# Optimization experiments

Measured on AMD Instinct MI355X. Metric: run time of the kernel, lower is better.

## Reference

```python
import jax, jax.numpy as jnp
import numpy as np

HIDDEN = 2048
NUM_HEADS = 16
NUM_KV_HEADS = 16
QK_NOPE = 128
QK_ROPE = 64
HEAD_DIM = QK_NOPE + QK_ROPE  # 192
V_HEAD = 128
KV_LORA = 512
Q_LORA = 1536
EPS = 1e-6


def rmsnorm(x, w):
    var = jnp.mean(x * x, axis=-1, keepdims=True)
    return x * jax.lax.rsqrt(var + EPS) * w


def setup_inputs() -> dict:
    key = jax.random.key(0)
    ks = jax.random.split(key, 8)
    s = lambda fan_in: 1.0 / np.sqrt(fan_in)
    return {
        "hidden_states": jax.random.normal(ks[0], (2, 2048, HIDDEN), jnp.float32),
        # weights stored as [in, out] so forward is x @ W
        "q_a_w": jax.random.normal(ks[1], (HIDDEN, Q_LORA), jnp.float32) * s(HIDDEN),
        "q_a_ln_w": jnp.ones((Q_LORA,), jnp.float32),
        "q_b_w": jax.random.normal(ks[2], (Q_LORA, NUM_HEADS * HEAD_DIM), jnp.float32) * s(Q_LORA),
        "kv_a_w": jax.random.normal(ks[3], (HIDDEN, KV_LORA + NUM_KV_HEADS * QK_ROPE), jnp.float32) * s(HIDDEN),
        "kv_a_ln_w": jnp.ones((KV_LORA,), jnp.float32),
        "kv_b_w": jax.random.normal(ks[4], (KV_LORA, NUM_KV_HEADS * (QK_NOPE + V_HEAD)), jnp.float32) * s(KV_LORA),
        "o_w": jax.random.normal(ks[5], (NUM_HEADS * V_HEAD, HIDDEN), jnp.float32) * s(NUM_HEADS * V_HEAD),
    }


def reference(hidden_states, q_a_w, q_a_ln_w, q_b_w, kv_a_w, kv_a_ln_w, kv_b_w, o_w):
    B, T, _ = hidden_states.shape
    # Q path: low-rank down-proj -> RMSNorm -> up-proj
    q = rmsnorm(hidden_states @ q_a_w, q_a_ln_w) @ q_b_w
    q = q.reshape(B, T, NUM_HEADS, HEAD_DIM)  # [B,T,H,192]

    # KV path: joint down-proj producing latent + rope slice
    kv_raw = hidden_states @ kv_a_w
    kv_latent = rmsnorm(kv_raw[..., :KV_LORA], kv_a_ln_w)
    k_rope = kv_raw[..., KV_LORA:].reshape(B, T, NUM_KV_HEADS, QK_ROPE)
    kv = (kv_latent @ kv_b_w).reshape(B, T, NUM_KV_HEADS, QK_NOPE + V_HEAD)
    k_nope = kv[..., :QK_NOPE]
    v = kv[..., QK_NOPE:]  # [B,T,Hkv,128]

    # NOTE: the original forward computes RoPE cos/sin but never applies the
    # rotation; q_rope/k_rope are used as-is (faithfully reproduced here).
    k = jnp.concatenate([k_nope, k_rope], axis=-1)  # [B,T,Hkv,192]
    # num_kv_groups == 1, so no repeat_interleave needed

    scale = 1.0 / jnp.sqrt(jnp.float32(HEAD_DIM))
    scores = jnp.einsum("bqhd,bkhd->bhqk", q, k) * scale  # [B,H,T,T]
    causal = jnp.tril(jnp.ones((T, T), bool))
    scores = jnp.where(causal, scores, jnp.finfo(scores.dtype).min)
    probs = jax.nn.softmax(scores, axis=-1)
    attn = jnp.einsum("bhqk,bkhd->bqhd", probs, v)  # [B,T,H,128]
    attn = attn.reshape(B, T, NUM_HEADS * V_HEAD)
    return attn @ o_w
```

## Files before the change

kernel.cpp:

```cpp
#include <hip/hip_runtime.h>
#include <cstdint>
#include <cstddef>

typedef unsigned short u16;
typedef short short8 __attribute__((ext_vector_type(8)));
typedef float f32x4 __attribute__((ext_vector_type(4)));

#define B_   2
#define T_   2048
#define H_   16
#define HID_ 2048
#define DQK_ 192
#define DV_  128
#define AW_  3072

__device__ __forceinline__ float bf2f(u16 u) {
  unsigned int v = ((unsigned int)u) << 16;
  return __builtin_bit_cast(float, v);
}
__device__ __forceinline__ u16 f2bf(float f) {
  unsigned int u = __builtin_bit_cast(unsigned int, f);
  u += 0x7fff + ((u >> 16) & 1);
  return (u16)(u >> 16);
}
__device__ __forceinline__ void load_lds16(const void* g, void* l) {
  __builtin_amdgcn_global_load_lds((const __attribute__((address_space(1))) void*)g,
                                   (__attribute__((address_space(3))) void*)l, 16, 0, 0);
}

__global__ __launch_bounds__(256) void cast_f32_bf16(const float* __restrict__ x,
                                                     u16* __restrict__ y) {
  size_t i = ((size_t)blockIdx.x * 256 + threadIdx.x) * 8;
  float4 a = *(const float4*)&x[i];
  float4 b = *(const float4*)&x[i + 4];
  u16 r[8];
  r[0] = f2bf(a.x); r[1] = f2bf(a.y); r[2] = f2bf(a.z); r[3] = f2bf(a.w);
  r[4] = f2bf(b.x); r[5] = f2bf(b.y); r[6] = f2bf(b.z); r[7] = f2bf(b.w);
  *(uint4*)&y[i] = *(const uint4*)&r[0];
}

__global__ __launch_bounds__(256) void transpose_cast_k(const float* __restrict__ W,
                                                        u16* __restrict__ Wt,
                                                        int K, int N) {
  __shared__ u16 tile[32][33];
  int n0 = blockIdx.x * 32, k0 = blockIdx.y * 32;
  int tx = threadIdx.x & 31, ty = threadIdx.x >> 5;
#pragma unroll
  for (int i = 0; i < 32; i += 8)
    tile[ty + i][tx] = f2bf(W[(size_t)(k0 + ty + i) * N + n0 + tx]);
  __syncthreads();
#pragma unroll
  for (int i = 0; i < 32; i += 8)
    Wt[(size_t)(n0 + ty + i) * K + k0 + tx] = tile[tx][ty + i];
}

__global__ __launch_bounds__(256) void rmsnorm_k(const u16* __restrict__ in, int in_stride,
                                                 int L, const float* __restrict__ w,
                                                 u16* __restrict__ out, int out_stride) {
  int row = blockIdx.x;
  const u16* x = in + (size_t)row * in_stride;
  float ss = 0.f;
  for (int i = threadIdx.x * 8; i < L; i += 2048) {
    uint4 v = *(const uint4*)&x[i];
    const u16* p = (const u16*)&v;
#pragma unroll
    for (int e = 0; e < 8; ++e) { float f = bf2f(p[e]); ss += f * f; }
  }
#pragma unroll
  for (int m = 32; m >= 1; m >>= 1) ss += __shfl_xor(ss, m);
  __shared__ float red[4];
  if ((threadIdx.x & 63) == 0) red[threadIdx.x >> 6] = ss;
  __syncthreads();
  ss = red[0] + red[1] + red[2] + red[3];
  float inv = rsqrtf(ss / (float)L + 1e-6f);
  u16* o = out + (size_t)row * out_stride;
  for (int i = threadIdx.x * 8; i < L; i += 2048) {
    uint4 v = *(const uint4*)&x[i];
    const u16* p = (const u16*)&v;
    u16 r8[8];
#pragma unroll
    for (int e = 0; e < 8; ++e) r8[e] = f2bf(bf2f(p[e]) * inv * w[i + e]);
    *(uint4*)&o[i] = *(const uint4*)&r8[0];
  }
}

template <int EPI>
__global__ __launch_bounds__(256) void gemm_bt(const u16* __restrict__ A,
                                               const u16* __restrict__ Bt,
                                               void* __restrict__ Cout,
                                               int M, int N, int K) {
  __shared__ u16 As[128 * 32];
  __shared__ u16 Bs[128 * 32];
  const int nbx = N >> 7;
  const int bx = blockIdx.x % nbx, by = blockIdx.x / nbx;
  const int m0 = by << 7, n0 = bx << 7;
  const int tid = threadIdx.x, w = tid >> 6, lane = tid & 63;
  const int wr = w >> 1, wc = w & 1;
  const int llo = lane & 15, lhi = lane >> 4;
  f32x4 acc[4][4] = {};
  const u16* Ag = A + (size_t)(m0 + w * 32 + (lane >> 2)) * K + (lane & 3) * 8;
  const u16* Bg = Bt + (size_t)(n0 + w * 32 + (lane >> 2)) * K + (lane & 3) * 8;
  u16* Al = &As[(w * 32 + (lane >> 2)) * 32 + (lane & 3) * 8];
  u16* Bl = &Bs[(w * 32 + (lane >> 2)) * 32 + (lane & 3) * 8];
  for (int k0 = 0; k0 < K; k0 += 32) {
    load_lds16(Ag + k0, Al);
    load_lds16(Ag + k0 + (size_t)16 * K, Al + 16 * 32);
    load_lds16(Bg + k0, Bl);
    load_lds16(Bg + k0 + (size_t)16 * K, Bl + 16 * 32);
    __syncthreads();
    short8 af[4], bfr[4];
#pragma unroll
    for (int i = 0; i < 4; ++i)
      af[i] = *(const short8*)&As[(wr * 64 + i * 16 + llo) * 32 + lhi * 8];
#pragma unroll
    for (int j = 0; j < 4; ++j)
      bfr[j] = *(const short8*)&Bs[(wc * 64 + j * 16 + llo) * 32 + lhi * 8];
#pragma unroll
    for (int i = 0; i < 4; ++i)
#pragma unroll
      for (int j = 0; j < 4; ++j)
        acc[i][j] = __builtin_amdgcn_mfma_f32_16x16x32_bf16(af[i], bfr[j], acc[i][j], 0, 0, 0);
    __syncthreads();
  }
  if constexpr (EPI == 0) {
    float* C = (float*)Cout;
#pragma unroll
    for (int i = 0; i < 4; ++i)
#pragma unroll
      for (int j = 0; j < 4; ++j)
#pragma unroll
        for (int r = 0; r < 4; ++r)
          C[(size_t)(m0 + wr * 64 + i * 16 + lhi * 4 + r) * N + (n0 + wc * 64 + j * 16 + llo)] =
              acc[i][j][r];
  } else {
    const float scale = (EPI == 3) ? 0.10412163f : 1.0f;
    u16* C = (u16*)Cout;
#pragma unroll
    for (int i = 0; i < 4; ++i)
#pragma unroll
      for (int j = 0; j < 4; ++j)
#pragma unroll
        for (int r = 0; r < 4; ++r)
          C[(size_t)(m0 + wr * 64 + i * 16 + lhi * 4 + r) * N + (n0 + wc * 64 + j * 16 + llo)] =
              f2bf(acc[i][j][r] * scale);
  }
}

__global__ __launch_bounds__(256) void pack_vt_k(const u16* __restrict__ kv, u16* __restrict__ Vt) {
  __shared__ u16 tile[64][136];
  const int nt = T_ / 64;
  int t0 = (blockIdx.x % nt) * 64;
  int bh = blockIdx.x / nt;
  int b = bh >> 4, h = bh & 15;
  int row = threadIdx.x >> 4;
  int ck = threadIdx.x & 15;
#pragma unroll
  for (int i = 0; i < 64; i += 16) {
    uint4 v = *(const uint4*)&kv[((size_t)(b * T_) + t0 + row + i) * 4096 + h * 256 + 128 + ck * 8];
    *(uint4*)&tile[row + i][ck * 8] = v;
  }
  __syncthreads();
  int d = threadIdx.x >> 1;
  int th = (threadIdx.x & 1) * 32;
  u16 tmp[32];
#pragma unroll
  for (int e = 0; e < 32; ++e) tmp[e] = tile[th + e][d];
#pragma unroll
  for (int e = 0; e < 32; e += 8)
    *(uint4*)&Vt[((size_t)bh * 128 + d) * T_ + t0 + th + e] = *(const uint4*)&tmp[e];
}

__global__ __launch_bounds__(256, 2) void attn_k(const u16* __restrict__ q,
                                                 const u16* __restrict__ kv,
                                                 const u16* __restrict__ kvraw,
                                                 const u16* __restrict__ Vt,
                                                 u16* __restrict__ att) {
  constexpr int KLD = 192, VLD = 64, PLD = 64;
  __shared__ u16 Ks[2][64 * KLD];
  __shared__ u16 Vs[128 * VLD];
  __shared__ u16 Ps[64 * PLD];
  const int idx = (int)blockIdx.x;
  const int bh = idx >> 4, pr = idx & 15;
  const int b = bh >> 4, h = bh & 15;
  const int bT = b * T_;
  const int tid = threadIdx.x, w = tid >> 6, lane = tid & 63;
  const int llo = lane & 15, lhi = lane >> 4;
  const u16* Vb = Vt + (size_t)bh * DV_ * T_;

  const u16* kbase[6]; int kstr[6];
#pragma unroll
  for (int ii = 0; ii < 6; ++ii) {
    int c = ii * 256 + tid;
    int rr = c / 24, chk = c - rr * 24;
    int sc = chk ^ (rr & 7);
    if (sc < 16) { kbase[ii] = kv + (size_t)(bT + rr) * 4096 + h * 256 + sc * 8; kstr[ii] = 4096; }
    else { kbase[ii] = kvraw + (size_t)(bT + rr) * AW_ + 2048 + h * 64 + (sc - 16) * 8; kstr[ii] = AW_; }
  }
  int voff[4];
#pragma unroll
  for (int ii = 0; ii < 4; ++ii) {
    int c = ii * 256 + tid;
    int rr = c >> 3, chk = c & 7;
    voff[ii] = rr * T_ + (chk ^ (rr & 7)) * 8;
  }

#pragma unroll
  for (int pass = 0; pass < 2; ++pass) {
    const int qt = pass == 0 ? 31 - pr : pr;
    const int q0 = qt * 64;
    const int rbase = q0 + w * 16;
    short8 qf[6];
#pragma unroll
    for (int kk = 0; kk < 6; ++kk)
      qf[kk] = *(const short8*)&q[(size_t)(bT + rbase + llo) * AW_ + h * DQK_ + kk * 32 + lhi * 8];
    f32x4 oacc[8] = {};
    float m_r[4], l_r[4];
#pragma unroll
    for (int r = 0; r < 4; ++r) { m_r[r] = -1e30f; l_r[r] = 0.f; }

#pragma unroll
    for (int ii = 0; ii < 6; ++ii)
      load_lds16(kbase[ii], &Ks[0][(ii * 256 + tid) * 8]);
    asm volatile("s_waitcnt vmcnt(0)" ::: "memory");
    __builtin_amdgcn_s_barrier();
    __builtin_amdgcn_sched_barrier(0);

    const int nkt = qt + 1;
    int cur = 0;
    for (int kt = 0; kt < nkt; ++kt) {
      const int k0 = kt * 64;
      const bool hasNext = (kt + 1 < nkt);
#pragma unroll
      for (int ii = 0; ii < 4; ++ii)
        load_lds16(Vb + k0 + voff[ii], &Vs[(ii * 256 + tid) * 8]);
      if (hasNext) {
        u16* kd = Ks[cur ^ 1];
#pragma unroll
        for (int ii = 0; ii < 6; ++ii)
          load_lds16(kbase[ii] + (size_t)(k0 + 64) * kstr[ii], &kd[(ii * 256 + tid) * 8]);
      }
      const u16* kbuf = Ks[cur];
      f32x4 s[4] = {};
      __builtin_amdgcn_s_setprio(1);
#pragma unroll
      for (int kk = 0; kk < 6; ++kk) {
        const int col = kk * 32 + lhi * 8;
        short8 kf[4];
#pragma unroll
        for (int j = 0; j < 4; ++j) {
          const int row = j * 16 + llo;
          kf[j] = *(const short8*)&kbuf[row * KLD + (col ^ ((row & 7) << 3))];
        }
#pragma unroll
        for (int j = 0; j < 4; ++j)
          s[j] = __builtin_amdgcn_mfma_f32_16x16x32_bf16(qf[kk], kf[j], s[j], 0, 0, 0);
      }
      __builtin_amdgcn_s_setprio(0);
      const bool needMask = (k0 + 63 > rbase);
#pragma unroll
      for (int r = 0; r < 4; ++r) {
        const int qrow = rbase + lhi * 4 + r;
        float sv[4];
#pragma unroll
        for (int j = 0; j < 4; ++j) {
          float x = s[j][r];
          if (needMask) { int kcol = k0 + j * 16 + llo; x = (kcol <= qrow) ? x : -1e30f; }
          sv[j] = x;
        }
        float mx = fmaxf(fmaxf(sv[0], sv[1]), fmaxf(sv[2], sv[3]));
#pragma unroll
        for (int mk = 1; mk < 16; mk <<= 1) mx = fmaxf(mx, __shfl_xor(mx, mk));
        if (!__all(mx - m_r[r] <= 8.f)) {
          float mnew = fmaxf(m_r[r], mx);
          float alpha = exp2f(m_r[r] - mnew);
          m_r[r] = mnew;
          l_r[r] *= alpha;
#pragma unroll
          for (int jo = 0; jo < 8; ++jo) oacc[jo][r] *= alpha;
        }
        float rs = 0.f;
        const int prow = w * 16 + lhi * 4 + r;
#pragma unroll
        for (int j = 0; j < 4; ++j) {
          float p = exp2f(sv[j] - m_r[r]);
          rs += p;
          int pcol = j * 16 + llo;
          Ps[prow * PLD + (pcol ^ ((prow & 7) << 3))] = f2bf(p);
        }
        l_r[r] += rs;
      }
      if (hasNext) asm volatile("s_waitcnt vmcnt(6)" ::: "memory");
      else         asm volatile("s_waitcnt vmcnt(0)" ::: "memory");
      __builtin_amdgcn_s_barrier();
      __builtin_amdgcn_sched_barrier(0);
      __builtin_amdgcn_s_setprio(1);
#pragma unroll
      for (int kk2 = 0; kk2 < 2; ++kk2) {
        const int prow = w * 16 + llo;
        const int pcol = kk2 * 32 + lhi * 8;
        short8 pf = *(const short8*)&Ps[prow * PLD + (pcol ^ ((prow & 7) << 3))];
#pragma unroll
        for (int jo = 0; jo < 8; ++jo) {
          const int vrow = jo * 16 + llo;
          short8 vf = *(const short8*)&Vs[vrow * VLD + (pcol ^ ((vrow & 7) << 3))];
          oacc[jo] = __builtin_amdgcn_mfma_f32_16x16x32_bf16(pf, vf, oacc[jo], 0, 0, 0);
        }
      }
      __builtin_amdgcn_s_setprio(0);
      asm volatile("s_waitcnt vmcnt(0)" ::: "memory");
      __builtin_amdgcn_s_barrier();
      __builtin_amdgcn_sched_barrier(0);
      cur ^= 1;
    }
#pragma unroll
    for (int r = 0; r < 4; ++r) {
      float lr = l_r[r];
#pragma unroll
      for (int mk = 1; mk < 16; mk <<= 1) lr += __shfl_xor(lr, mk);
      const int qrow = rbase + lhi * 4 + r;
      const float linv = 1.f / lr;
#pragma unroll
      for (int jo = 0; jo < 8; ++jo)
        att[((size_t)bT + qrow) * (H_ * DV_) + h * DV_ + jo * 16 + llo] =
            f2bf(oacc[jo][r] * linv);
    }
  }
}

extern "C" void kernel_launch(void* const* d_in, const int* in_sizes, int n_in,
                              void* d_out, int out_size, void* d_ws, size_t ws_size,
                              hipStream_t stream) {
  const float* hs      = (const float*)d_in[0];
  const float* q_a_w   = (const float*)d_in[1];
  const float* q_a_ln  = (const float*)d_in[2];
  const float* q_b_w   = (const float*)d_in[3];
  const float* kv_a_w  = (const float*)d_in[4];
  const float* kv_a_ln = (const float*)d_in[5];
  const float* kv_b_w  = (const float*)d_in[6];
  const float* o_w     = (const float*)d_in[7];
  float* out = (float*)d_out;
  char* ws = (char*)d_ws;

  u16* hid  = (u16*)(ws + 0);
  u16* wt   = (u16*)(ws + 16777216);
  u16* qa   = (u16*)(ws + 29360128);
  u16* qan  = (u16*)(ws + 54525952);
  u16* qout = (u16*)(ws + 67108864);
  u16* att  = (u16*)(ws + 92274688);
  u16* kv   = (u16*)(ws + 109051904);
  u16* Vt   = (u16*)(ws + 142606336);

  cast_f32_bf16<<<4096, 256, 0, stream>>>(hs, hid);

  transpose_cast_k<<<dim3(1536 / 32, 2048 / 32), 256, 0, stream>>>(q_a_w, wt, 2048, 1536);
  transpose_cast_k<<<dim3(1536 / 32, 2048 / 32), 256, 0, stream>>>(kv_a_w, wt + (size_t)1536 * 2048, 2048, 1536);
  gemm_bt<1><<<(3072 / 128) * (4096 / 128), 256, 0, stream>>>(hid, wt, qa, 4096, 3072, 2048);

  rmsnorm_k<<<4096, 256, 0, stream>>>(qa, AW_, 1536, q_a_ln, qan, 1536);

  transpose_cast_k<<<dim3(3072 / 32, 1536 / 32), 256, 0, stream>>>(q_b_w, wt, 1536, 3072);
  gemm_bt<3><<<(3072 / 128) * (4096 / 128), 256, 0, stream>>>(qan, wt, qout, 4096, 3072, 1536);

  rmsnorm_k<<<4096, 256, 0, stream>>>(qa + 1536, AW_, 512, kv_a_ln, qan, 512);

  transpose_cast_k<<<dim3(4096 / 32, 512 / 32), 256, 0, stream>>>(kv_b_w, wt, 512, 4096);
  gemm_bt<1><<<(4096 / 128) * (4096 / 128), 256, 0, stream>>>(qan, wt, kv, 4096, 4096, 512);

  pack_vt_k<<<1024, 256, 0, stream>>>(kv, Vt);

  attn_k<<<512, 256, 0, stream>>>(qout, kv, qa, Vt, att);

  transpose_cast_k<<<dim3(2048 / 32, 2048 / 32), 256, 0, stream>>>(o_w, wt, 2048, 2048);
  gemm_bt<0><<<(2048 / 128) * (4096 / 128), 256, 0, stream>>>(att, wt, out, 4096, 2048, 2048);
}
```

Before: 380.9 us.

## Triple-buffer GEMM LDS tiles with XOR swizzle and async prefetch

The bf16 GEMM kernel now uses three LDS stage buffers and prefetches tiles two k-steps ahead using direct-to-LDS loads. Manual vmcnt waits with one barrier per iteration replace the two syncthreads. An XOR swizzle on the LDS layout targets bank conflicts in the MFMA fragment reads. The MFMA block also gets raised wave priority. This triples LDS per block, which can reduce occupancy, and the hand-written waitcnt logic risks races if the load count assumptions are wrong.

```diff
diff --git a/kernel.cpp b/kernel.cpp
--- a/kernel.cpp
+++ b/kernel.cpp
@@ -89,8 +89,8 @@
                                                const u16* __restrict__ Bt,
                                                void* __restrict__ Cout,
                                                int M, int N, int K) {
-  __shared__ u16 As[128 * 32];
-  __shared__ u16 Bs[128 * 32];
+  __shared__ u16 As[3][128 * 32];
+  __shared__ u16 Bs[3][128 * 32];
   const int nbx = N >> 7;
   const int bx = blockIdx.x % nbx, by = blockIdx.x / nbx;
   const int m0 = by << 7, n0 = bx << 7;
@@ -98,30 +98,62 @@
   const int wr = w >> 1, wc = w & 1;
   const int llo = lane & 15, lhi = lane >> 4;
   f32x4 acc[4][4] = {};
-  const u16* Ag = A + (size_t)(m0 + w * 32 + (lane >> 2)) * K + (lane & 3) * 8;
-  const u16* Bg = Bt + (size_t)(n0 + w * 32 + (lane >> 2)) * K + (lane & 3) * 8;
-  u16* Al = &As[(w * 32 + (lane >> 2)) * 32 + (lane & 3) * 8];
-  u16* Bl = &Bs[(w * 32 + (lane >> 2)) * 32 + (lane & 3) * 8];
-  for (int k0 = 0; k0 < K; k0 += 32) {
-    load_lds16(Ag + k0, Al);
-    load_lds16(Ag + k0 + (size_t)16 * K, Al + 16 * 32);
-    load_lds16(Bg + k0, Bl);
-    load_lds16(Bg + k0 + (size_t)16 * K, Bl + 16 * 32);
-    __syncthreads();
+
+  const int c0 = tid, c1 = tid + 256;
+  const int ar0 = c0 >> 2, s0_ = c0 & 3;
+  const int ar1 = c1 >> 2, s1_ = c1 & 3;
+  const u16* Asrc0 = A + (size_t)(m0 + ar0) * K + (s0_ ^ ((ar0 >> 1) & 3)) * 8;
+  const u16* Asrc1 = A + (size_t)(m0 + ar1) * K + (s1_ ^ ((ar1 >> 1) & 3)) * 8;
+  const u16* Bsrc0 = Bt + (size_t)(n0 + ar0) * K + (s0_ ^ ((ar0 >> 1) & 3)) * 8;
+  const u16* Bsrc1 = Bt + (size_t)(n0 + ar1) * K + (s1_ ^ ((ar1 >> 1) & 3)) * 8;
+
+  int aoff[4], boff[4];
+#pragma unroll
+  for (int i = 0; i < 4; ++i) {
+    int rowa = wr * 64 + i * 16 + llo;
+    aoff[i] = (rowa * 4 + (lhi ^ ((rowa >> 1) & 3))) * 8;
+    int rowb = wc * 64 + i * 16 + llo;
+    boff[i] = (rowb * 4 + (lhi ^ ((rowb >> 1) & 3))) * 8;
+  }
+
+#define STAGE_KT(kt, buf)                                   \
+  do {                                                      \
+    int k0_ = (kt) << 5;                                    \
+    load_lds16(Asrc0 + k0_, &As[(buf)][c0 * 8]);            \
+    load_lds16(Asrc1 + k0_, &As[(buf)][c1 * 8]);            \
+    load_lds16(Bsrc0 + k0_, &Bs[(buf)][c0 * 8]);            \
+    load_lds16(Bsrc1 + k0_, &Bs[(buf)][c1 * 8]);            \
+  } while (0)
+
+  const int NT = K >> 5;
+  STAGE_KT(0, 0);
+  STAGE_KT(1, 1);
+  asm volatile("s_waitcnt vmcnt(4)" ::: "memory");
+  __builtin_amdgcn_s_barrier();
+
+  int cur = 0, nxt = 2;
+  for (int kt = 0; kt < NT; ++kt) {
+    if (kt + 2 < NT) STAGE_KT(kt + 2, nxt);
     short8 af[4], bfr[4];
 #pragma unroll
-    for (int i = 0; i < 4; ++i)
-      af[i] = *(const short8*)&As[(wr * 64 + i * 16 + llo) * 32 + lhi * 8];
-#pragma unroll
-    for (int j = 0; j < 4; ++j)
-      bfr[j] = *(const short8*)&Bs[(wc * 64 + j * 16 + llo) * 32 + lhi * 8];
+    for (int i = 0; i < 4; ++i) af[i] = *(const short8*)&As[cur][aoff[i]];
+#pragma unroll
+    for (int j = 0; j < 4; ++j) bfr[j] = *(const short8*)&Bs[cur][boff[j]];
+    __builtin_amdgcn_s_setprio(1);
 #pragma unroll
     for (int i = 0; i < 4; ++i)
 #pragma unroll
       for (int j = 0; j < 4; ++j)
         acc[i][j] = __builtin_amdgcn_mfma_f32_16x16x32_bf16(af[i], bfr[j], acc[i][j], 0, 0, 0);
-    __syncthreads();
-  }
+    __builtin_amdgcn_s_setprio(0);
+    if (kt + 2 < NT) asm volatile("s_waitcnt vmcnt(4)" ::: "memory");
+    else             asm volatile("s_waitcnt vmcnt(0)" ::: "memory");
+    __builtin_amdgcn_s_barrier();
+    cur = (cur == 2) ? 0 : cur + 1;
+    nxt = (nxt == 2) ? 0 : nxt + 1;
+  }
+#undef STAGE_KT
+
   if constexpr (EPI == 0) {
     float* C = (float*)Cout;
 #pragma unroll
```

Result: faster. 366.0 us (-3.9%).
